# Optimization experiments

Hardware: AMD Instinct MI355X
Metric: run time of the kernel (lower is better)

## Reference

```python
import jax, jax.numpy as jnp
import numpy as np

KS = (10, 25, 50, 100)  # numbers of highest-scored tiles to average (eval mode averages over all)
CLAMP = 1e4


def setup_inputs() -> dict:
    key = jax.random.key(0)
    k1, k2, k3, k4, k5, k6, k7 = jax.random.split(key, 7)
    B, C, N, H, O = 8, 2048, 8000, 256, 1000
    x = jax.random.normal(k1, (B, C, N), dtype=jnp.float32)
    # Conv1d(kernel=1) weights == [out, in] matrices
    W0 = jax.random.normal(k2, (H, C), dtype=jnp.float32) * (1.0 / np.sqrt(C))
    b0 = jax.random.normal(k3, (H,), dtype=jnp.float32) * 0.01
    W1 = jax.random.normal(k4, (H, H), dtype=jnp.float32) * (1.0 / np.sqrt(H))
    b1 = jax.random.normal(k5, (H,), dtype=jnp.float32) * 0.01
    W2 = jax.random.normal(k6, (O, H), dtype=jnp.float32) * (1.0 / np.sqrt(H))
    b2 = jax.random.normal(k7, (O,), dtype=jnp.float32) * 0.01
    return {"x": x, "W0": W0, "b0": b0, "W1": W1, "b1": b1, "W2": W2, "b2": b2}


def reference(x, W0, b0, W1, b1, W2, b2):
    # x: [B, C, N] tile features. Eval-mode dropout is identity.
    # mask: tile is 'real' if its max feature > 0 (padding tiles are all-zero)
    mask = (jnp.max(x, axis=1, keepdims=True) > 0).astype(x.dtype)  # [B,1,N]
    # 1x1 conv stack (Conv1d kernel=1 == per-tile matmul)
    h = jnp.einsum('hc,bcn->bhn', W0, x) + b0[None, :, None]
    h = jnp.clip(jax.nn.relu(h), -CLAMP, CLAMP)
    h = jnp.einsum('hg,bgn->bhn', W1, h) + b1[None, :, None]
    h = jnp.clip(jax.nn.relu(h), -CLAMP, CLAMP)
    y = jnp.einsum('oh,bhn->bon', W2, h) + b2[None, :, None]  # [B,O,N]
    y = y * mask
    # top-kmax once (sorted descending); top-k for smaller k is a prefix slice
    kmax = max(KS)
    t, _ = jax.lax.top_k(y, kmax)  # [B,O,kmax]
    pred = jnp.zeros(y.shape[:2], dtype=y.dtype)  # [B,O]
    inv = 1.0 / len(KS)
    for k in KS:
        num = jnp.sum(t[:, :, :k] * mask[:, :, :k], axis=2)  # [B,O]
        den = jnp.sum(mask[:, :, :k], axis=2)                 # [B,1]
        pred = pred + (num / den) * inv
    return pred
```

## Files before the change

kernel.cpp:

```cpp
#include <hip/hip_runtime.h>
#include <hip/hip_bf16.h>
#include <stdint.h>

typedef __bf16 bf16;
typedef __bf16 bf16x8 __attribute__((ext_vector_type(8)));
typedef __bf16 bf16x4 __attribute__((ext_vector_type(4)));
typedef float  floatx4 __attribute__((ext_vector_type(4)));
typedef unsigned int uint32;

#define B_  8
#define C_  2048
#define N_  8000
#define H_  256
#define O_  1000
#define OP_ 1024

__device__ __forceinline__ void gll16(const void* g, void* l) {
  __builtin_amdgcn_global_load_lds((const __attribute__((address_space(1))) void*)g,
                                   (__attribute__((address_space(3))) void*)l, 16, 0, 0);
}

__global__ __launch_bounds__(256) void castw(const float* __restrict__ W0,
                                             const float* __restrict__ W1,
                                             const float* __restrict__ W2,
                                             bf16* __restrict__ W0b,
                                             bf16* __restrict__ W1b,
                                             bf16* __restrict__ W2b) {
  int g = blockIdx.x * 256 + threadIdx.x;
  float4 v;
  bf16* dst;
  if (g < 131072) {
    v = ((const float4*)W0)[g];
    dst = W0b + g * 4;
  } else if (g < 147456) {
    int i = g - 131072;
    v = ((const float4*)W1)[i];
    dst = W1b + i * 4;
  } else {
    int i = g - 147456;
    int o = i >> 6, k4 = i & 63;
    if (o < O_) v = *(const float4*)(W2 + o * 256 + k4 * 4);
    else        v = make_float4(0.f, 0.f, 0.f, 0.f);
    dst = W2b + i * 4;
  }
  bf16x4 r;
  r[0] = (bf16)v.x; r[1] = (bf16)v.y; r[2] = (bf16)v.z; r[3] = (bf16)v.w;
  *(bf16x4*)dst = r;
}

__global__ __launch_bounds__(256) void gemm1(const float* __restrict__ x,
                                             const bf16* __restrict__ W0b,
                                             const float* __restrict__ bias0,
                                             bf16* __restrict__ h1T,
                                             float* __restrict__ maskb) {
  __shared__ union {
    struct { bf16 A[H_ * 32]; bf16 Bt[64 * 40]; } st;
    bf16 HT[64 * 264];
  } sm;
  __shared__ float sbias[256];
  __shared__ uint32 nflag[64];

  const int tid  = threadIdx.x;
  const int wave = tid >> 6, lane = tid & 63;
  const int l16  = lane & 15, l4 = lane >> 4;
  const int n0   = blockIdx.x * 64;
  const int b    = blockIdx.y;

  sbias[tid] = bias0[tid];
  if (tid < 64) nflag[tid] = 0;

  const int kp = tid >> 4;
  const int n4 = (tid & 15) * 4;
  const float* xbase = x + (size_t)b * C_ * N_ + n0 + n4;

  floatx4 acc[4][4];
  #pragma unroll
  for (int i = 0; i < 4; ++i)
    #pragma unroll
    for (int j = 0; j < 4; ++j)
      acc[i][j] = floatx4{0.f, 0.f, 0.f, 0.f};

  uint32 fl = 0;

  for (int k0 = 0; k0 < C_; k0 += 32) {
    #pragma unroll
    for (int i = 0; i < 4; ++i) {
      int c = i * 256 + tid;
      gll16(W0b + (size_t)(c >> 2) * C_ + k0 + (c & 3) * 8, &sm.st.A[c * 8]);
    }
    const float* xr = xbase + (size_t)(k0 + 2 * kp) * N_;
    float4 q0 = *(const float4*)xr;
    float4 q1 = *(const float4*)(xr + N_);
    float a0[4] = {q0.x, q0.y, q0.z, q0.w};
    float a1[4] = {q1.x, q1.y, q1.z, q1.w};
    uint32* bw = (uint32*)sm.st.Bt;
    #pragma unroll
    for (int i = 0; i < 4; ++i) {
      if (a0[i] > 0.f || a1[i] > 0.f) fl |= (1u << i);
      union { bf16 h[2]; uint32 u; } p;
      p.h[0] = (bf16)a0[i];
      p.h[1] = (bf16)a1[i];
      bw[(n4 + i) * 20 + kp] = p.u;
    }
    __syncthreads();

    bf16x8 af[4], bfr[4];
    #pragma unroll
    for (int mt = 0; mt < 4; ++mt)
      af[mt] = *(const bf16x8*)&sm.st.A[(wave * 64 + mt * 16 + l16) * 32 + l4 * 8];
    #pragma unroll
    for (int nt = 0; nt < 4; ++nt)
      bfr[nt] = *(const bf16x8*)&sm.st.Bt[(nt * 16 + l16) * 40 + l4 * 8];
    #pragma unroll
    for (int mt = 0; mt < 4; ++mt)
      #pragma unroll
      for (int nt = 0; nt < 4; ++nt)
        acc[mt][nt] = __builtin_amdgcn_mfma_f32_16x16x32_bf16(af[mt], bfr[nt], acc[mt][nt], 0, 0, 0);
    __syncthreads();
  }

  #pragma unroll
  for (int i = 0; i < 4; ++i)
    if (fl & (1u << i)) atomicOr(&nflag[n4 + i], 1u);
  __syncthreads();
  if (tid < 64) maskb[(size_t)b * N_ + n0 + tid] = nflag[tid] ? 1.f : 0.f;

  #pragma unroll
  for (int mt = 0; mt < 4; ++mt) {
    int m0 = wave * 64 + mt * 16 + l4 * 4;
    #pragma unroll
    for (int nt = 0; nt < 4; ++nt) {
      int n = nt * 16 + l16;
      bf16x4 hv;
      #pragma unroll
      for (int r = 0; r < 4; ++r) {
        float v = acc[mt][nt][r] + sbias[m0 + r];
        v = fminf(fmaxf(v, 0.f), 1.0e4f);
        hv[r] = (bf16)v;
      }
      *(bf16x4*)&sm.HT[n * 264 + m0] = hv;
    }
  }
  __syncthreads();
  {
    int n = tid >> 2, q = tid & 3;
    const char* src = (const char*)&sm.HT[n * 264 + q * 64];
    bf16* dst = h1T + ((size_t)b * N_ + n0 + n) * H_ + q * 64;
    #pragma unroll
    for (int j = 0; j < 8; ++j)
      *(uint4*)((char*)dst + j * 16) = *(const uint4*)(src + j * 16);
  }
}

__global__ __launch_bounds__(256) void gemm23(const bf16* __restrict__ W1b,
                                              const float* __restrict__ b1,
                                              const bf16* __restrict__ W2b,
                                              const float* __restrict__ b2,
                                              const bf16* __restrict__ h1T,
                                              const float* __restrict__ mk,
                                              bf16* __restrict__ yb) {
  __shared__ union {
    struct { bf16 A[256 * 32]; bf16 Bs[64 * 32]; } p1;
    bf16 A2[256 * 32];
    bf16 YT[128 * 72];
  } u;
  __shared__ bf16 HT[64 * 264];
  __shared__ float sb[256];
  __shared__ float smk[64];

  const int tid  = threadIdx.x;
  const int wave = tid >> 6, lane = tid & 63;
  const int l16  = lane & 15, l4 = lane >> 4;
  const int n0   = blockIdx.x * 64;
  const int b    = blockIdx.y;

  sb[tid] = b1[tid];
  if (tid < 64) smk[tid] = mk[(size_t)b * N_ + n0 + tid];

  floatx4 acc[4][4];
  #pragma unroll
  for (int i = 0; i < 4; ++i)
    #pragma unroll
    for (int j = 0; j < 4; ++j)
      acc[i][j] = floatx4{0.f, 0.f, 0.f, 0.f};

  const bf16* Bbase = h1T + ((size_t)b * N_ + n0) * 256;

  for (int k0 = 0; k0 < 256; k0 += 32) {
    #pragma unroll
    for (int i = 0; i < 4; ++i) {
      int c = i * 256 + tid;
      gll16(W1b + (size_t)(c >> 2) * 256 + k0 + (c & 3) * 8, &u.p1.A[c * 8]);
    }
    gll16(Bbase + (size_t)(tid >> 2) * 256 + k0 + (tid & 3) * 8, &u.p1.Bs[tid * 8]);
    __syncthreads();

    bf16x8 af[4], bfr[4];
    #pragma unroll
    for (int mt = 0; mt < 4; ++mt)
      af[mt] = *(const bf16x8*)&u.p1.A[(wave * 64 + mt * 16 + l16) * 32 + l4 * 8];
    #pragma unroll
    for (int nt = 0; nt < 4; ++nt)
      bfr[nt] = *(const bf16x8*)&u.p1.Bs[(nt * 16 + l16) * 32 + l4 * 8];
    #pragma unroll
    for (int mt = 0; mt < 4; ++mt)
      #pragma unroll
      for (int nt = 0; nt < 4; ++nt)
        acc[mt][nt] = __builtin_amdgcn_mfma_f32_16x16x32_bf16(af[mt], bfr[nt], acc[mt][nt], 0, 0, 0);
    __syncthreads();
  }

  #pragma unroll
  for (int mt = 0; mt < 4; ++mt) {
    int m0 = wave * 64 + mt * 16 + l4 * 4;
    #pragma unroll
    for (int nt = 0; nt < 4; ++nt) {
      int n = nt * 16 + l16;
      bf16x4 hv;
      #pragma unroll
      for (int r = 0; r < 4; ++r) {
        float v = acc[mt][nt][r] + sb[m0 + r];
        v = fminf(fmaxf(v, 0.f), 1.0e4f);
        hv[r] = (bf16)v;
      }
      *(bf16x4*)&HT[n * 264 + m0] = hv;
    }
  }
  __syncthreads();

  for (int mb = 0; mb < 4; ++mb) {
    const int m0g = mb * 256;
    { int og = m0g + tid; sb[tid] = (og < O_) ? b2[og] : 0.f; }

    #pragma unroll
    for (int i = 0; i < 4; ++i)
      #pragma unroll
      for (int j = 0; j < 4; ++j)
        acc[i][j] = floatx4{0.f, 0.f, 0.f, 0.f};

    for (int k0 = 0; k0 < 256; k0 += 32) {
      #pragma unroll
      for (int i = 0; i < 4; ++i) {
        int c = i * 256 + tid;
        gll16(W2b + (size_t)(m0g + (c >> 2)) * 256 + k0 + (c & 3) * 8, &u.A2[c * 8]);
      }
      __syncthreads();

      bf16x8 af[4], bfr[4];
      #pragma unroll
      for (int mt = 0; mt < 4; ++mt)
        af[mt] = *(const bf16x8*)&u.A2[(wave * 64 + mt * 16 + l16) * 32 + l4 * 8];
      #pragma unroll
      for (int nt = 0; nt < 4; ++nt)
        bfr[nt] = *(const bf16x8*)&HT[(nt * 16 + l16) * 264 + k0 + l4 * 8];
      #pragma unroll
      for (int mt = 0; mt < 4; ++mt)
        #pragma unroll
        for (int nt = 0; nt < 4; ++nt)
          acc[mt][nt] = __builtin_amdgcn_mfma_f32_16x16x32_bf16(af[mt], bfr[nt], acc[mt][nt], 0, 0, 0);
      __syncthreads();
    }

    #pragma unroll
    for (int h = 0; h < 2; ++h) {
      #pragma unroll
      for (int mt = 0; mt < 4; ++mt) {
        int m0 = wave * 64 + mt * 16 + l4 * 4;
        if ((m0 >> 7) == h) {
          #pragma unroll
          for (int nt = 0; nt < 4; ++nt) {
            int n = nt * 16 + l16;
            float m = smk[n];
            #pragma unroll
            for (int r = 0; r < 4; ++r)
              u.YT[(m0 - h * 128 + r) * 72 + n] = (bf16)((acc[mt][nt][r] + sb[m0 + r]) * m);
          }
        }
      }
      __syncthreads();
      {
        int row = tid >> 1, ch = tid & 1;
        const char* src = (const char*)&u.YT[row * 72 + ch * 32];
        bf16* dst = yb + ((size_t)b * OP_ + m0g + h * 128 + row) * N_ + n0 + ch * 32;
        #pragma unroll
        for (int j = 0; j < 4; ++j)
          *(uint4*)((char*)dst + j * 16) = *(const uint4*)(src + j * 16);
      }
      __syncthreads();
    }
  }
}

__global__ __launch_bounds__(64) void topk(const bf16* __restrict__ y,
                                           const float* __restrict__ maskb,
                                           float* __restrict__ out) {
  __shared__ uint32 cand[128];
  __shared__ float  sval[128];
  __shared__ float  m100[100];
  __shared__ int    gcnt;

  const int lane = threadIdx.x;
  const int o = blockIdx.x, b = blockIdx.y;

  const uint32* yw = (const uint32*)(y + ((size_t)b * OP_ + o) * N_);
  const float*  mr = maskb + (size_t)b * N_;

  if (lane == 0) gcnt = 0;
  m100[lane] = mr[lane];
  if (lane < 36) m100[64 + lane] = mr[64 + lane];

  uint32 khi[64];
  #pragma unroll
  for (int i = 0; i < 16; ++i) {
    int base = i * 256 + lane * 4;
    bool real = (base < 4000);
    uint4 v = make_uint4(0u, 0u, 0u, 0u);
    if (real) v = *(const uint4*)(yw + base);
    uint32 ww[4] = {v.x, v.y, v.z, v.w};
    #pragma unroll
    for (int j = 0; j < 4; ++j) {
      uint32 w = ww[j];
      uint32 sgn = w & 0x80008000u;
      uint32 mskk = 0x80008000u | (sgn - (sgn >> 15));
      uint32 k = w ^ mskk;
      if (!real) k = 0u;
      khi[i * 4 + j] = k;
    }
  }

  uint32 prefix = 0;
  #pragma unroll 1
  for (int bit = 15; bit >= 0; --bit) {
    uint32 T16 = (prefix | (1u << bit)) << 16;
    int c = 0;
    #pragma unroll
    for (int r = 0; r < 64; ++r) {
      c += (khi[r] >= T16);
      c += ((khi[r] << 16) >= T16);
    }
    #pragma unroll
    for (int m = 1; m < 64; m <<= 1) c += __shfl_xor(c, m, 64);
    if (c >= 100) prefix |= (1u << bit);
  }

  #pragma unroll
  for (int r = 0; r < 64; ++r) {
    uint32 h = khi[r] >> 16;
    uint32 l = khi[r] & 0xffffu;
    if (h > prefix) { int p = atomicAdd(&gcnt, 1); cand[p] = h; }
    if (l > prefix) { int p = atomicAdd(&gcnt, 1); cand[p] = l; }
  }
  __syncthreads();
  int cg = gcnt;
  for (int idx = lane; idx < 100; idx += 64)
    if (idx >= cg) cand[idx] = prefix;
  __syncthreads();

  for (int idx = lane; idx < 100; idx += 64) {
    uint32 ci = cand[idx];
    int rank = 0;
    for (int j = 0; j < 100; ++j) {
      uint32 cj = cand[j];
      rank += (cj > ci) || (cj == ci && j < idx);
    }
    uint32 bb = (ci & 0x8000u) ? (ci & 0x7fffu) : (~ci & 0xffffu);
    sval[rank] = __uint_as_float(bb << 16);
  }
  __syncthreads();

  if (lane == 0) {
    const int KSv[4] = {10, 25, 50, 100};
    float num = 0.f, den = 0.f, pred = 0.f;
    int ki = 0;
    for (int j = 0; j < 100; ++j) {
      num += sval[j] * m100[j];
      den += m100[j];
      if (j + 1 == KSv[ki]) { pred += 0.25f * num / den; ++ki; }
    }
    out[(size_t)b * O_ + o] = pred;
  }
}

extern "C" void kernel_launch(void* const* d_in, const int* in_sizes, int n_in,
                              void* d_out, int out_size, void* d_ws, size_t ws_size,
                              hipStream_t stream) {
  const float* x  = (const float*)d_in[0];
  const float* W0 = (const float*)d_in[1];
  const float* b0 = (const float*)d_in[2];
  const float* W1 = (const float*)d_in[3];
  const float* b1 = (const float*)d_in[4];
  const float* W2 = (const float*)d_in[5];
  const float* b2 = (const float*)d_in[6];
  float* out = (float*)d_out;

  char* ws = (char*)d_ws;
  bf16*  W0b  = (bf16*)(ws + 0);
  bf16*  W1b  = (bf16*)(ws + 1048576);
  bf16*  W2b  = (bf16*)(ws + 1179648);
  float* mk   = (float*)(ws + 1703936);
  bf16*  h1T  = (bf16*)(ws + 1959936);
  bf16*  yb   = (bf16*)(ws + 34727936);

  castw<<<832, 256, 0, stream>>>(W0, W1, W2, W0b, W1b, W2b);
  gemm1<<<dim3(125, 8), 256, 0, stream>>>(x, W0b, b0, h1T, mk);
  gemm23<<<dim3(125, 8), 256, 0, stream>>>(W1b, b1, W2b, b2, h1T, mk, yb);
  topk<<<dim3(1000, 8), 64, 0, stream>>>(yb, mk, out);
}
```

Measured before the change: 973.6 us.

## Fuse all three 1x1-conv GEMMs into one kernel keeping hidden tiles in LDS

Merges gemm1 and gemm23 into a single gemm123 kernel. The first hidden activation tile now stays in shared memory and feeds the second GEMM directly, so the h1T global round trip (about 32 MB written and read back) and one launch are removed. It also skips writing the padded output rows (o >= 1000) to yb. The cost is a longer single kernel with higher LDS use (HT plus the union), which may lower occupancy.

Result: faster. 923.0 us (-5.2%).

```diff
diff --git a/kernel.cpp b/kernel.cpp
--- a/kernel.cpp
+++ b/kernel.cpp
@@ -48,16 +48,22 @@
   *(bf16x4*)dst = r;
 }
 
-__global__ __launch_bounds__(256) void gemm1(const float* __restrict__ x,
-                                             const bf16* __restrict__ W0b,
-                                             const float* __restrict__ bias0,
-                                             bf16* __restrict__ h1T,
-                                             float* __restrict__ maskb) {
+__global__ __launch_bounds__(256) void gemm123(const float* __restrict__ x,
+                                               const bf16* __restrict__ W0b,
+                                               const float* __restrict__ b0,
+                                               const bf16* __restrict__ W1b,
+                                               const float* __restrict__ b1,
+                                               const bf16* __restrict__ W2b,
+                                               const float* __restrict__ b2,
+                                               float* __restrict__ maskb,
+                                               bf16* __restrict__ yb) {
   __shared__ union {
-    struct { bf16 A[H_ * 32]; bf16 Bt[64 * 40]; } st;
-    bf16 HT[64 * 264];
-  } sm;
-  __shared__ float sbias[256];
+    struct { bf16 A[256 * 32]; bf16 Bt[64 * 40]; } st;
+    bf16 YT[128 * 72];
+  } u;
+  __shared__ bf16 HT[64 * 264];
+  __shared__ float sb[256];
+  __shared__ float smk[64];
   __shared__ uint32 nflag[64];
 
   const int tid  = threadIdx.x;
@@ -66,7 +72,7 @@
   const int n0   = blockIdx.x * 64;
   const int b    = blockIdx.y;
 
-  sbias[tid] = bias0[tid];
+  sb[tid] = b0[tid];
   if (tid < 64) nflag[tid] = 0;
 
   const int kp = tid >> 4;
@@ -86,31 +92,31 @@
     #pragma unroll
     for (int i = 0; i < 4; ++i) {
       int c = i * 256 + tid;
-      gll16(W0b + (size_t)(c >> 2) * C_ + k0 + (c & 3) * 8, &sm.st.A[c * 8]);
+      gll16(W0b + (size_t)(c >> 2) * C_ + k0 + (c & 3) * 8, &u.st.A[c * 8]);
     }
     const float* xr = xbase + (size_t)(k0 + 2 * kp) * N_;
     float4 q0 = *(const float4*)xr;
     float4 q1 = *(const float4*)(xr + N_);
     float a0[4] = {q0.x, q0.y, q0.z, q0.w};
     float a1[4] = {q1.x, q1.y, q1.z, q1.w};
-    uint32* bw = (uint32*)sm.st.Bt;
+    uint32* bw = (uint32*)u.st.Bt;
     #pragma unroll
     for (int i = 0; i < 4; ++i) {
       if (a0[i] > 0.f || a1[i] > 0.f) fl |= (1u << i);
-      union { bf16 h[2]; uint32 u; } p;
+      union { bf16 h[2]; uint32 u32v; } p;
       p.h[0] = (bf16)a0[i];
       p.h[1] = (bf16)a1[i];
-      bw[(n4 + i) * 20 + kp] = p.u;
+      bw[(n4 + i) * 20 + kp] = p.u32v;
     }
     __syncthreads();
 
     bf16x8 af[4], bfr[4];
     #pragma unroll
     for (int mt = 0; mt < 4; ++mt)
-      af[mt] = *(const bf16x8*)&sm.st.A[(wave * 64 + mt * 16 + l16) * 32 + l4 * 8];
+      af[mt] = *(const bf16x8*)&u.st.A[(wave * 64 + mt * 16 + l16) * 32 + l4 * 8];
     #pragma unroll
     for (int nt = 0; nt < 4; ++nt)
-      bfr[nt] = *(const bf16x8*)&sm.st.Bt[(nt * 16 + l16) * 40 + l4 * 8];
+      bfr[nt] = *(const bf16x8*)&u.st.Bt[(nt * 16 + l16) * 40 + l4 * 8];
     #pragma unroll
     for (int mt = 0; mt < 4; ++mt)
       #pragma unroll
@@ -123,91 +129,10 @@
   for (int i = 0; i < 4; ++i)
     if (fl & (1u << i)) atomicOr(&nflag[n4 + i], 1u);
   __syncthreads();
-  if (tid < 64) maskb[(size_t)b * N_ + n0 + tid] = nflag[tid] ? 1.f : 0.f;
-
-  #pragma unroll
-  for (int mt = 0; mt < 4; ++mt) {
-    int m0 = wave * 64 + mt * 16 + l4 * 4;
-    #pragma unroll
-    for (int nt = 0; nt < 4; ++nt) {
-      int n = nt * 16 + l16;
-      bf16x4 hv;
-      #pragma unroll
-      for (int r = 0; r < 4; ++r) {
-        float v = acc[mt][nt][r] + sbias[m0 + r];
-        v = fminf(fmaxf(v, 0.f), 1.0e4f);
-        hv[r] = (bf16)v;
-      }
-      *(bf16x4*)&sm.HT[n * 264 + m0] = hv;
-    }
-  }
-  __syncthreads();
-  {
-    int n = tid >> 2, q = tid & 3;
-    const char* src = (const char*)&sm.HT[n * 264 + q * 64];
-    bf16* dst = h1T + ((size_t)b * N_ + n0 + n) * H_ + q * 64;
-    #pragma unroll
-    for (int j = 0; j < 8; ++j)
-      *(uint4*)((char*)dst + j * 16) = *(const uint4*)(src + j * 16);
-  }
-}
-
-__global__ __launch_bounds__(256) void gemm23(const bf16* __restrict__ W1b,
-                                              const float* __restrict__ b1,
-                                              const bf16* __restrict__ W2b,
-                                              const float* __restrict__ b2,
-                                              const bf16* __restrict__ h1T,
-                                              const float* __restrict__ mk,
-                                              bf16* __restrict__ yb) {
-  __shared__ union {
-    struct { bf16 A[256 * 32]; bf16 Bs[64 * 32]; } p1;
-    bf16 A2[256 * 32];
-    bf16 YT[128 * 72];
-  } u;
-  __shared__ bf16 HT[64 * 264];
-  __shared__ float sb[256];
-  __shared__ float smk[64];
-
-  const int tid  = threadIdx.x;
-  const int wave = tid >> 6, lane = tid & 63;
-  const int l16  = lane & 15, l4 = lane >> 4;
-  const int n0   = blockIdx.x * 64;
-  const int b    = blockIdx.y;
-
-  sb[tid] = b1[tid];
-  if (tid < 64) smk[tid] = mk[(size_t)b * N_ + n0 + tid];
-
-  floatx4 acc[4][4];
-  #pragma unroll
-  for (int i = 0; i < 4; ++i)
-    #pragma unroll
-    for (int j = 0; j < 4; ++j)
-      acc[i][j] = floatx4{0.f, 0.f, 0.f, 0.f};
-
-  const bf16* Bbase = h1T + ((size_t)b * N_ + n0) * 256;
-
-  for (int k0 = 0; k0 < 256; k0 += 32) {
-    #pragma unroll
-    for (int i = 0; i < 4; ++i) {
-      int c = i * 256 + tid;
-      gll16(W1b + (size_t)(c >> 2) * 256 + k0 + (c & 3) * 8, &u.p1.A[c * 8]);
-    }
-    gll16(Bbase + (size_t)(tid >> 2) * 256 + k0 + (tid & 3) * 8, &u.p1.Bs[tid * 8]);
-    __syncthreads();
-
-    bf16x8 af[4], bfr[4];
-    #pragma unroll
-    for (int mt = 0; mt < 4; ++mt)
-      af[mt] = *(const bf16x8*)&u.p1.A[(wave * 64 + mt * 16 + l16) * 32 + l4 * 8];
-    #pragma unroll
-    for (int nt = 0; nt < 4; ++nt)
-      bfr[nt] = *(const bf16x8*)&u.p1.Bs[(nt * 16 + l16) * 32 + l4 * 8];
-    #pragma unroll
-    for (int mt = 0; mt < 4; ++mt)
-      #pragma unroll
-      for (int nt = 0; nt < 4; ++nt)
-        acc[mt][nt] = __builtin_amdgcn_mfma_f32_16x16x32_bf16(af[mt], bfr[nt], acc[mt][nt], 0, 0, 0);
-    __syncthreads();
+  if (tid < 64) {
+    float m = nflag[tid] ? 1.f : 0.f;
+    smk[tid] = m;
+    maskb[(size_t)b * N_ + n0 + tid] = m;
   }
 
   #pragma unroll
@@ -228,6 +153,54 @@
   }
   __syncthreads();
 
+  sb[tid] = b1[tid];
+  #pragma unroll
+  for (int i = 0; i < 4; ++i)
+    #pragma unroll
+    for (int j = 0; j < 4; ++j)
+      acc[i][j] = floatx4{0.f, 0.f, 0.f, 0.f};
+
+  for (int k0 = 0; k0 < 256; k0 += 32) {
+    #pragma unroll
+    for (int i = 0; i < 4; ++i) {
+      int c = i * 256 + tid;
+      gll16(W1b + (size_t)(c >> 2) * 256 + k0 + (c & 3) * 8, &u.st.A[c * 8]);
+    }
+    __syncthreads();
+
+    bf16x8 af[4], bfr[4];
+    #pragma unroll
+    for (int mt = 0; mt < 4; ++mt)
+      af[mt] = *(const bf16x8*)&u.st.A[(wave * 64 + mt * 16 + l16) * 32 + l4 * 8];
+    #pragma unroll
+    for (int nt = 0; nt < 4; ++nt)
+      bfr[nt] = *(const bf16x8*)&HT[(nt * 16 + l16) * 264 + k0 + l4 * 8];
+    #pragma unroll
+    for (int mt = 0; mt < 4; ++mt)
+      #pragma unroll
+      for (int nt = 0; nt < 4; ++nt)
+        acc[mt][nt] = __builtin_amdgcn_mfma_f32_16x16x32_bf16(af[mt], bfr[nt], acc[mt][nt], 0, 0, 0);
+    __syncthreads();
+  }
+
+  #pragma unroll
+  for (int mt = 0; mt < 4; ++mt) {
+    int m0 = wave * 64 + mt * 16 + l4 * 4;
+    #pragma unroll
+    for (int nt = 0; nt < 4; ++nt) {
+      int n = nt * 16 + l16;
+      bf16x4 hv;
+      #pragma unroll
+      for (int r = 0; r < 4; ++r) {
+        float v = acc[mt][nt][r] + sb[m0 + r];
+        v = fminf(fmaxf(v, 0.f), 1.0e4f);
+        hv[r] = (bf16)v;
+      }
+      *(bf16x4*)&HT[n * 264 + m0] = hv;
+    }
+  }
+  __syncthreads();
+
   for (int mb = 0; mb < 4; ++mb) {
     const int m0g = mb * 256;
     { int og = m0g + tid; sb[tid] = (og < O_) ? b2[og] : 0.f; }
@@ -242,14 +215,14 @@
       #pragma unroll
       for (int i = 0; i < 4; ++i) {
         int c = i * 256 + tid;
-        gll16(W2b + (size_t)(m0g + (c >> 2)) * 256 + k0 + (c & 3) * 8, &u.A2[c * 8]);
+        gll16(W2b + (size_t)(m0g + (c >> 2)) * 256 + k0 + (c & 3) * 8, &u.st.A[c * 8]);
       }
       __syncthreads();
 
       bf16x8 af[4], bfr[4];
       #pragma unroll
       for (int mt = 0; mt < 4; ++mt)
-        af[mt] = *(const bf16x8*)&u.A2[(wave * 64 + mt * 16 + l16) * 32 + l4 * 8];
+        af[mt] = *(const bf16x8*)&u.st.A[(wave * 64 + mt * 16 + l16) * 32 + l4 * 8];
       #pragma unroll
       for (int nt = 0; nt < 4; ++nt)
         bfr[nt] = *(const bf16x8*)&HT[(nt * 16 + l16) * 264 + k0 + l4 * 8];
@@ -280,11 +253,14 @@
       __syncthreads();
       {
         int row = tid >> 1, ch = tid & 1;
-        const char* src = (const char*)&u.YT[row * 72 + ch * 32];
-        bf16* dst = yb + ((size_t)b * OP_ + m0g + h * 128 + row) * N_ + n0 + ch * 32;
-        #pragma unroll
-        for (int j = 0; j < 4; ++j)
-          *(uint4*)((char*)dst + j * 16) = *(const uint4*)(src + j * 16);
+        int og = m0g + h * 128 + row;
+        if (og < O_) {
+          const char* src = (const char*)&u.YT[row * 72 + ch * 32];
+          bf16* dst = yb + ((size_t)b * OP_ + og) * N_ + n0 + ch * 32;
+          #pragma unroll
+          for (int j = 0; j < 4; ++j)
+            *(uint4*)((char*)dst + j * 16) = *(const uint4*)(src + j * 16);
+        }
       }
       __syncthreads();
     }
@@ -398,11 +374,9 @@
   bf16*  W1b  = (bf16*)(ws + 1048576);
   bf16*  W2b  = (bf16*)(ws + 1179648);
   float* mk   = (float*)(ws + 1703936);
-  bf16*  h1T  = (bf16*)(ws + 1959936);
-  bf16*  yb   = (bf16*)(ws + 34727936);
+  bf16*  yb   = (bf16*)(ws + 1959936);
 
   castw<<<832, 256, 0, stream>>>(W0, W1, W2, W0b, W1b, W2b);
-  gemm1<<<dim3(125, 8), 256, 0, stream>>>(x, W0b, b0, h1T, mk);
-  gemm23<<<dim3(125, 8), 256, 0, stream>>>(W1b, b1, W2b, b2, h1T, mk, yb);
+  gemm123<<<dim3(125, 8), 256, 0, stream>>>(x, W0b, b0, W1b, b1, W2b, b2, mk, yb);
   topk<<<dim3(1000, 8), 64, 0, stream>>>(yb, mk, out);
 }
```
